# Performance work log

Hardware: AMD Instinct MI355X
Metric: run time of the kernel (lower is better)

The kernel has to match this reference:

```python
import jax, jax.numpy as jnp
import numpy as np

N = 50000
E = 800000
D_IN = 64
D_H = 64


def setup_inputs() -> dict:
    key = jax.random.key(0)
    k1, k2, k3, k4 = jax.random.split(key, 4)
    x = jax.random.normal(k1, (N, D_IN), dtype=jnp.float32)
    edge_index = jax.random.randint(k2, (2, E), 0, N, dtype=jnp.int32)
    W1 = jax.random.normal(k3, (D_IN, D_H), dtype=jnp.float32) * (1.0 / np.sqrt(D_IN))
    b1 = jnp.zeros((D_H,), dtype=jnp.float32)
    W2 = jax.random.normal(k4, (D_H, 1), dtype=jnp.float32) * (1.0 / np.sqrt(D_H))
    b2 = jnpp = jnp.zeros((1,), dtype=jnp.float32)
    return {"x": x, "edge_index": edge_index, "W1": W1, "b1": b1, "W2": W2, "b2": b2}


def reference(x, edge_index, W1, b1, W2, b2):
    n = x.shape[0]
    # dgl.add_self_loop: append (i, i) edges for every node
    loops = jnp.arange(n, dtype=edge_index.dtype)
    src = jnp.concatenate([edge_index[0], loops])
    dst = jnp.concatenate([edge_index[1], loops])

    ones = jnp.ones(src.shape[0], dtype=x.dtype)
    deg_out = jax.ops.segment_sum(ones, src, num_segments=n)  # out-degree (src side)
    deg_in = jax.ops.segment_sum(ones, dst, num_segments=n)   # in-degree (dst side)
    # norm='both': symmetric D^{-1/2} A D^{-1/2}; zero where degree is zero (DGL sets inf->0)
    norm_src = jnp.where(deg_out > 0, jax.lax.rsqrt(deg_out), 0.0)[:, None]
    norm_dst = jnp.where(deg_in > 0, jax.lax.rsqrt(deg_in), 0.0)[:, None]

    def aggregate(h):
        # degree-normalized sparse neighbor sum (SpMM via gather + segment_sum)
        h = h * norm_src
        m = jax.ops.segment_sum(h[src], dst, num_segments=n)
        return m * norm_dst

    # layer 1 (in_feats == h_feats -> aggregate first, then transform), bias after agg
    h = aggregate(x) @ W1 + b1
    h = jax.nn.relu(h)
    # layer 2 (in_feats > out_feats -> transform first, then aggregate), bias at end
    out = aggregate(h @ W2) + b2
    return out  # [N, 1]
```

## Files before the change

kernel.cpp:

```cpp
#include <hip/hip_runtime.h>


constexpr int D = 64;
constexpr int NODE_TILE = 12800;
constexpr int NCHUNK = 64;
constexpr int HTH = 1024;

typedef float f32x8 __attribute__((ext_vector_type(8)));

__device__ __forceinline__ int rl_i(int v, int l) { return __builtin_amdgcn_readlane(v, l); }
__device__ __forceinline__ float rl_f(float v, int l) {
    return __builtin_bit_cast(float, __builtin_amdgcn_readlane(__builtin_bit_cast(int, v), l));
}

__global__ void __launch_bounds__(HTH) k_hist_gemm(
        const int* __restrict__ src, const int* __restrict__ dst,
        unsigned int* __restrict__ part, int e, int ce, int hblocks,
        const float* __restrict__ x, const float* __restrict__ W1,
        float* __restrict__ y, int n) {
    extern __shared__ char smem[];
    int tid = threadIdx.x;

    if (blockIdx.x < (unsigned)hblocks) {
        unsigned int* h = (unsigned int*)smem;
        int b = blockIdx.x & (NCHUNK - 1);
        int pass = blockIdx.x >> 6;
        int v0 = pass * NODE_TILE;
        for (int i = tid; i < NODE_TILE; i += HTH) h[i] = 0u;
        __syncthreads();
        int lo = b * ce, hi = min(lo + ce, e);
        for (int i = lo + tid; i < hi; i += HTH) {
            unsigned int us = (unsigned int)(src[i] - v0);
            if (us < (unsigned int)NODE_TILE) atomicAdd(&h[us], 1u);
            unsigned int ud = (unsigned int)(dst[i] - v0);
            if (ud < (unsigned int)NODE_TILE) atomicAdd(&h[ud], 0x10000u);
        }
        __syncthreads();
        unsigned int* p = part + ((size_t)pass * NCHUNK + b) * NODE_TILE;
        for (int i = tid; i < NODE_TILE; i += HTH) p[i] = h[i];
    } else {
        float* sW1 = (float*)smem;
        for (int i = tid; i < D * D; i += HTH) sW1[i] = W1[i];
        __syncthreads();

        int lane = tid & 63;
        int wv = __builtin_amdgcn_readfirstlane(tid >> 6);
        int gb = blockIdx.x - hblocks;
        int r0 = (gb * 16 + wv) * 8;
        if (r0 >= n) return;

        float acc[8];
#pragma unroll
        for (int i = 0; i < 8; ++i) acc[i] = 0.0f;

        if (r0 + 8 <= n) {
            const float* xw = x + (size_t)r0 * D;
#pragma unroll
            for (int kt = 0; kt < 8; ++kt) {
                const float* p = xw + kt * 8;
                f32x8 X0, X1, X2, X3, X4, X5, X6, X7;
                asm volatile(
                    "s_load_dwordx8 %0, %8, 0x0\n\t"
                    "s_load_dwordx8 %1, %8, 0x100\n\t"
                    "s_load_dwordx8 %2, %8, 0x200\n\t"
                    "s_load_dwordx8 %3, %8, 0x300\n\t"
                    "s_load_dwordx8 %4, %8, 0x400\n\t"
                    "s_load_dwordx8 %5, %8, 0x500\n\t"
                    "s_load_dwordx8 %6, %8, 0x600\n\t"
                    "s_load_dwordx8 %7, %8, 0x700\n\t"
                    "s_waitcnt lgkmcnt(0)"
                    : "=s"(X0), "=s"(X1), "=s"(X2), "=s"(X3),
                      "=s"(X4), "=s"(X5), "=s"(X6), "=s"(X7)
                    : "s"(p));
#pragma unroll
                for (int j = 0; j < 8; ++j) {
                    float wk = sW1[(kt * 8 + j) * D + lane];
                    acc[0] = fmaf(X0[j], wk, acc[0]);
                    acc[1] = fmaf(X1[j], wk, acc[1]);
                    acc[2] = fmaf(X2[j], wk, acc[2]);
                    acc[3] = fmaf(X3[j], wk, acc[3]);
                    acc[4] = fmaf(X4[j], wk, acc[4]);
                    acc[5] = fmaf(X5[j], wk, acc[5]);
                    acc[6] = fmaf(X6[j], wk, acc[6]);
                    acc[7] = fmaf(X7[j], wk, acc[7]);
                }
            }
#pragma unroll
            for (int i = 0; i < 8; ++i)
                y[(size_t)(r0 + i) * D + lane] = acc[i];
        } else {
            float xr[8];
#pragma unroll
            for (int i = 0; i < 8; ++i) {
                int r = r0 + i;
                xr[i] = (r < n) ? x[(size_t)r * D + lane] : 0.0f;
            }
#pragma unroll
            for (int k = 0; k < D; ++k) {
                float wk = sW1[k * D + lane];
#pragma unroll
                for (int i = 0; i < 8; ++i)
                    acc[i] = fmaf(rl_f(xr[i], k), wk, acc[i]);
            }
#pragma unroll
            for (int i = 0; i < 8; ++i) {
                int r = r0 + i;
                if (r < n) y[(size_t)r * D + lane] = acc[i];
            }
        }
    }
}

__global__ void k_merge_scan(const unsigned int* __restrict__ part,
                             unsigned short* __restrict__ colpref,
                             int* __restrict__ cnt_out, int* __restrict__ cnt_in,
                             int* __restrict__ cursor, int* __restrict__ bsum, int n) {
    __shared__ int s[256];
    int tid = threadIdx.x;
    int v = blockIdx.x * 256 + tid;
    int ci = 0;
    if (v < n) {
        int pass = v / NODE_TILE;
        int vl = v - pass * NODE_TILE;
        const unsigned int* p = part + (size_t)pass * NCHUNK * NODE_TILE + vl;
        unsigned int tot = 0, run_in = 0;
        for (int b = 0; b < NCHUNK; ++b) {
            colpref[(size_t)b * n + v] = (unsigned short)run_in;
            unsigned int t = p[(size_t)b * NODE_TILE];
            tot += t;
            run_in += t >> 16;
        }
        cnt_out[v] = (int)(tot & 0xFFFFu);
        ci = (int)(tot >> 16);
        cnt_in[v] = ci;
    }
    s[tid] = ci;
    __syncthreads();
#pragma unroll
    for (int off = 1; off < 256; off <<= 1) {
        int t = (tid >= off) ? s[tid - off] : 0;
        __syncthreads();
        s[tid] += t;
        __syncthreads();
    }
    if (v < n) cursor[v] = s[tid] - ci;
    if (tid == 255) bsum[blockIdx.x] = s[255];
}

__global__ void k_scan_bsum(int* __restrict__ bsum, int nb) {
    __shared__ int s[256];
    __shared__ int carry;
    int tid = threadIdx.x;
    if (tid == 0) carry = 0;
    __syncthreads();
    for (int start = 0; start < nb; start += 256) {
        int i = start + tid;
        int v = (i < nb) ? bsum[i] : 0;
        s[tid] = v;
        __syncthreads();
#pragma unroll
        for (int off = 1; off < 256; off <<= 1) {
            int t = (tid >= off) ? s[tid - off] : 0;
            __syncthreads();
            s[tid] += t;
            __syncthreads();
        }
        if (i < nb) bsum[i] = s[tid] - v + carry;
        __syncthreads();
        if (tid == 0) carry += s[255];
        __syncthreads();
    }
}

__global__ void __launch_bounds__(HTH) k_bin_lds(
        const int* __restrict__ src, const int* __restrict__ dst,
        const int* __restrict__ cursor, const int* __restrict__ bsum,
        const unsigned short* __restrict__ colpref,
        const int* __restrict__ cnt_out, const int* __restrict__ cnt_in,
        unsigned int* __restrict__ col, int4* __restrict__ meta,
        int e, int n, int ce) {
    __shared__ int cur[NODE_TILE];
    int b = blockIdx.x;
    int v0 = blockIdx.y * NODE_TILE;
    int vcnt = min(NODE_TILE, n - v0);
    for (int i = threadIdx.x; i < vcnt; i += HTH) {
        int v = v0 + i;
        int gs = cursor[v] + bsum[v >> 8];
        cur[i] = gs + (int)colpref[(size_t)b * n + v];
        if (b == 0) meta[v] = make_int4(gs, cnt_in[v], cnt_out[v], 0);
    }
    __syncthreads();
    int lo = b * ce, hi = min(lo + ce, e);
    for (int i = lo + threadIdx.x; i < hi; i += HTH) {
        int d = dst[i];
        unsigned int ud = (unsigned int)(d - v0);
        if (ud < (unsigned int)NODE_TILE) {
            int s = src[i];
            int p = atomicAdd(&cur[ud], 1);
            col[p] = (unsigned int)s | ((unsigned int)cnt_out[s] << 16);
        }
    }
}

__global__ void __launch_bounds__(256) k_node(
        const float* __restrict__ y, const int4* __restrict__ meta,
        const unsigned int* __restrict__ col,
        const float* __restrict__ b1, const float* __restrict__ W2,
        float* __restrict__ zs, int n) {
    int tid = threadIdx.x;
    int wave = tid >> 6;
    int lane = tid & 63;
    float b1v = b1[lane];
    float w2v = W2[lane];

    int nwaves = gridDim.x * 4;
    int node = blockIdx.x * 4 + wave;
    if (node >= n) return;
    int4 mt = meta[node];

    while (true) {
        int nxt = node + nwaves;
        int4 mt_nx = make_int4(0, 0, 0, 0);
        if (nxt < n) mt_nx = meta[nxt];

        int base = mt.x;
        int cnt = mt.y;
        float nd = rsqrtf((float)(mt.y + 1));
        float ns = rsqrtf((float)(mt.z + 1));

        float a0 = ns * y[(size_t)node * D + lane];
        float a1 = 0.0f, a2 = 0.0f, a3 = 0.0f;

        for (int b0 = 0; b0 < cnt; b0 += 64) {
            int m = cnt - b0; if (m > 64) m = 64;
            unsigned int cw = (lane < m) ? col[base + b0 + lane] : 0u;
            int idx = (int)(cw & 0xFFFFu);
            float w = rsqrtf((float)(cw >> 16) + 1.0f);
            int j = 0;
            for (; j + 8 <= m; j += 8) {
                int s0 = rl_i(idx, j + 0), s1 = rl_i(idx, j + 1);
                int s2 = rl_i(idx, j + 2), s3 = rl_i(idx, j + 3);
                int s4 = rl_i(idx, j + 4), s5 = rl_i(idx, j + 5);
                int s6 = rl_i(idx, j + 6), s7 = rl_i(idx, j + 7);
                float x0 = y[(size_t)s0 * D + lane];
                float x1 = y[(size_t)s1 * D + lane];
                float x2 = y[(size_t)s2 * D + lane];
                float x3 = y[(size_t)s3 * D + lane];
                float x4 = y[(size_t)s4 * D + lane];
                float x5 = y[(size_t)s5 * D + lane];
                float x6 = y[(size_t)s6 * D + lane];
                float x7 = y[(size_t)s7 * D + lane];
                a0 = fmaf(rl_f(w, j + 0), x0, a0);
                a1 = fmaf(rl_f(w, j + 1), x1, a1);
                a2 = fmaf(rl_f(w, j + 2), x2, a2);
                a3 = fmaf(rl_f(w, j + 3), x3, a3);
                a0 = fmaf(rl_f(w, j + 4), x4, a0);
                a1 = fmaf(rl_f(w, j + 5), x5, a1);
                a2 = fmaf(rl_f(w, j + 6), x6, a2);
                a3 = fmaf(rl_f(w, j + 7), x7, a3);
            }
            for (; j < m; ++j)
                a0 = fmaf(rl_f(w, j), y[(size_t)rl_i(idx, j) * D + lane], a0);
        }

        float h = fmaxf(((a0 + a1) + (a2 + a3)) * nd + b1v, 0.0f);
        float zp = h * w2v;
#pragma unroll
        for (int off = 32; off > 0; off >>= 1) zp += __shfl_down(zp, off);
        if (lane == 0) zs[node] = zp * ns;

        if (nxt >= n) break;
        node = nxt;
        mt = mt_nx;
    }
}

__global__ void k_out(const float* __restrict__ zs,
                      const int4* __restrict__ meta, const unsigned int* __restrict__ col,
                      const float* __restrict__ b2,
                      float* __restrict__ out, int n) {
    int g = blockIdx.x * blockDim.x + threadIdx.x;
    int node = g >> 3;
    int sub = g & 7;
    if (node >= n) return;
    int4 mt = meta[node];
    int base = mt.x;
    int c = mt.y;
    float s = (sub == 0) ? zs[node] : 0.0f;
    for (int j = sub; j < c; j += 8) s += zs[col[base + j] & 0xFFFFu];
    s += __shfl_xor(s, 1);
    s += __shfl_xor(s, 2);
    s += __shfl_xor(s, 4);
    if (sub == 0) {
        float nd = rsqrtf((float)(mt.y + 1));
        out[node] = nd * s + b2[0];
    }
}

extern "C" void kernel_launch(void* const* d_in, const int* in_sizes, int n_in,
                              void* d_out, int out_size, void* d_ws, size_t ws_size,
                              hipStream_t stream) {
    const float* x  = (const float*)d_in[0];
    const int*   ei = (const int*)d_in[1];
    const float* W1 = (const float*)d_in[2];
    const float* b1 = (const float*)d_in[3];
    const float* W2 = (const float*)d_in[4];
    const float* b2 = (const float*)d_in[5];
    float* out = (float*)d_out;

    const int n = in_sizes[0] / D;
    const int e = in_sizes[1] / 2;
    const int* src = ei;
    const int* dst = ei + e;

    const int nb = (n + 255) / 256;
    const int npass = (n + NODE_TILE - 1) / NODE_TILE;
    const int ce = (e + NCHUNK - 1) / NCHUNK;
    const int hblocks = NCHUNK * npass;
    const int gblocks = (n + 127) / 128;

    char* ws = (char*)d_ws;
    int*   cnt_out = (int*)ws;   ws += sizeof(int) * (size_t)n;
    int*   cnt_in  = (int*)ws;   ws += sizeof(int) * (size_t)n;
    int*   cursor  = (int*)ws;   ws += sizeof(int) * (size_t)n;
    int*   bsum    = (int*)ws;   ws += sizeof(int) * (size_t)((nb + 255) & ~255);
    int4*  meta    = (int4*)ws;  ws += sizeof(int4) * (size_t)n;
    unsigned short* colpref = (unsigned short*)ws;
    ws += sizeof(unsigned short) * (size_t)NCHUNK * n;
    unsigned int* col = (unsigned int*)ws;  ws += sizeof(unsigned int) * (size_t)e;
    unsigned int* part = (unsigned int*)ws;
    ws += sizeof(unsigned int) * (size_t)npass * NCHUNK * NODE_TILE;
    float* y  = (float*)ws;      ws += sizeof(float) * (size_t)n * D;
    float* zs = (float*)ws;      ws += sizeof(float) * (size_t)n;

    const int B = 256;
    const size_t smem = (size_t)NODE_TILE * sizeof(unsigned int);

    k_hist_gemm<<<hblocks + gblocks, HTH, smem, stream>>>(
        src, dst, part, e, ce, hblocks, x, W1, y, n);
    k_merge_scan<<<nb, 256, 0, stream>>>(part, colpref, cnt_out, cnt_in, cursor, bsum, n);
    k_scan_bsum<<<1, 256, 0, stream>>>(bsum, nb);
    k_bin_lds<<<dim3(NCHUNK, npass), HTH, 0, stream>>>(
        src, dst, cursor, bsum, colpref, cnt_out, cnt_in, col, meta, e, n, ce);
    k_node<<<2048, B, 0, stream>>>(y, meta, col, b1, W2, zs, n);
    k_out<<<((size_t)n * 8 + B - 1) / B, B, 0, stream>>>(zs, meta, col, b2, out, n);
}
```

Before: 105.6 us.

## Pack two nodes per 32-bit LDS histogram word to cover all nodes in one pass

The per-node histograms now hold two 16-bit counters per 32-bit LDS word, so all 50000 nodes fit in one block's shared memory (about 100KB). This removes the four-pass node tiling that made every chunk rescan all edges once per tile. In/out degree histograms move to separate block sets, and the binning kernel now runs as a single pass that also uses packed 16-bit cursors. The int4 meta array is dropped in favour of packed in/out counts plus cursor+bsum computed on the fly, which adds extra global loads in the node and output kernels and relies on per-chunk counts staying under 65536.

After: 118.1 us. +11.8%, slower.

```diff
diff --git a/kernel.cpp b/kernel.cpp
--- a/kernel.cpp
+++ b/kernel.cpp
@@ -2,7 +2,6 @@
 
 
 constexpr int D = 64;
-constexpr int NODE_TILE = 12800;
 constexpr int NCHUNK = 64;
 constexpr int HTH = 1024;
 
@@ -15,29 +14,28 @@
 
 __global__ void __launch_bounds__(HTH) k_hist_gemm(
         const int* __restrict__ src, const int* __restrict__ dst,
-        unsigned int* __restrict__ part, int e, int ce, int hblocks,
+        unsigned int* __restrict__ part_in, unsigned int* __restrict__ part_out,
+        int e, int ce, int W,
         const float* __restrict__ x, const float* __restrict__ W1,
         float* __restrict__ y, int n) {
-    extern __shared__ char smem[];
+    extern __shared__ unsigned int smem[];
     int tid = threadIdx.x;
 
-    if (blockIdx.x < (unsigned)hblocks) {
-        unsigned int* h = (unsigned int*)smem;
+    if (blockIdx.x < 2 * NCHUNK) {
+        unsigned int* h = smem;
+        int isOut = (blockIdx.x >= NCHUNK) ? 1 : 0;
         int b = blockIdx.x & (NCHUNK - 1);
-        int pass = blockIdx.x >> 6;
-        int v0 = pass * NODE_TILE;
-        for (int i = tid; i < NODE_TILE; i += HTH) h[i] = 0u;
+        const int* key = isOut ? src : dst;
+        for (int i = tid; i < W; i += HTH) h[i] = 0u;
         __syncthreads();
         int lo = b * ce, hi = min(lo + ce, e);
         for (int i = lo + tid; i < hi; i += HTH) {
-            unsigned int us = (unsigned int)(src[i] - v0);
-            if (us < (unsigned int)NODE_TILE) atomicAdd(&h[us], 1u);
-            unsigned int ud = (unsigned int)(dst[i] - v0);
-            if (ud < (unsigned int)NODE_TILE) atomicAdd(&h[ud], 0x10000u);
-        }
-        __syncthreads();
-        unsigned int* p = part + ((size_t)pass * NCHUNK + b) * NODE_TILE;
-        for (int i = tid; i < NODE_TILE; i += HTH) p[i] = h[i];
+            int v = key[i];
+            atomicAdd(&h[v >> 1], (v & 1) ? 0x10000u : 1u);
+        }
+        __syncthreads();
+        unsigned int* p = (isOut ? part_out : part_in) + (size_t)b * W;
+        for (int i = tid; i < W; i += HTH) p[i] = h[i];
     } else {
         float* sW1 = (float*)smem;
         for (int i = tid; i < D * D; i += HTH) sW1[i] = W1[i];
@@ -45,7 +43,7 @@
 
         int lane = tid & 63;
         int wv = __builtin_amdgcn_readfirstlane(tid >> 6);
-        int gb = blockIdx.x - hblocks;
+        int gb = blockIdx.x - 2 * NCHUNK;
         int r0 = (gb * 16 + wv) * 8;
         if (r0 >= n) return;
 
@@ -111,28 +109,27 @@
     }
 }
 
-__global__ void k_merge_scan(const unsigned int* __restrict__ part,
+__global__ void k_merge_scan(const unsigned int* __restrict__ part_in,
+                             const unsigned int* __restrict__ part_out,
                              unsigned short* __restrict__ colpref,
-                             int* __restrict__ cnt_out, int* __restrict__ cnt_in,
-                             int* __restrict__ cursor, int* __restrict__ bsum, int n) {
+                             unsigned int* __restrict__ cnts,
+                             int* __restrict__ cursor, int* __restrict__ bsum,
+                             int n, int W) {
     __shared__ int s[256];
     int tid = threadIdx.x;
     int v = blockIdx.x * 256 + tid;
     int ci = 0;
     if (v < n) {
-        int pass = v / NODE_TILE;
-        int vl = v - pass * NODE_TILE;
-        const unsigned int* p = part + (size_t)pass * NCHUNK * NODE_TILE + vl;
-        unsigned int tot = 0, run_in = 0;
+        int sh = (v & 1) * 16;
+        size_t w = (size_t)(v >> 1);
+        unsigned int run_in = 0, tout = 0;
         for (int b = 0; b < NCHUNK; ++b) {
             colpref[(size_t)b * n + v] = (unsigned short)run_in;
-            unsigned int t = p[(size_t)b * NODE_TILE];
-            tot += t;
-            run_in += t >> 16;
-        }
-        cnt_out[v] = (int)(tot & 0xFFFFu);
-        ci = (int)(tot >> 16);
-        cnt_in[v] = ci;
+            run_in += (part_in[(size_t)b * W + w] >> sh) & 0xFFFFu;
+            tout   += (part_out[(size_t)b * W + w] >> sh) & 0xFFFFu;
+        }
+        ci = (int)run_in;
+        cnts[v] = run_in | (tout << 16);
     }
     s[tid] = ci;
     __syncthreads();
@@ -172,38 +169,32 @@
     }
 }
 
-__global__ void __launch_bounds__(HTH) k_bin_lds(
+__global__ void __launch_bounds__(HTH) k_bin(
         const int* __restrict__ src, const int* __restrict__ dst,
         const int* __restrict__ cursor, const int* __restrict__ bsum,
         const unsigned short* __restrict__ colpref,
-        const int* __restrict__ cnt_out, const int* __restrict__ cnt_in,
-        unsigned int* __restrict__ col, int4* __restrict__ meta,
-        int e, int n, int ce) {
-    __shared__ int cur[NODE_TILE];
+        const unsigned int* __restrict__ cnts,
+        unsigned int* __restrict__ col, int e, int n, int ce, int W) {
+    extern __shared__ unsigned int cur[];
     int b = blockIdx.x;
-    int v0 = blockIdx.y * NODE_TILE;
-    int vcnt = min(NODE_TILE, n - v0);
-    for (int i = threadIdx.x; i < vcnt; i += HTH) {
-        int v = v0 + i;
-        int gs = cursor[v] + bsum[v >> 8];
-        cur[i] = gs + (int)colpref[(size_t)b * n + v];
-        if (b == 0) meta[v] = make_int4(gs, cnt_in[v], cnt_out[v], 0);
-    }
+    const unsigned int* cp = (const unsigned int*)(colpref + (size_t)b * n);
+    for (int i = threadIdx.x; i < W; i += HTH) cur[i] = cp[i];
     __syncthreads();
     int lo = b * ce, hi = min(lo + ce, e);
     for (int i = lo + threadIdx.x; i < hi; i += HTH) {
         int d = dst[i];
-        unsigned int ud = (unsigned int)(d - v0);
-        if (ud < (unsigned int)NODE_TILE) {
-            int s = src[i];
-            int p = atomicAdd(&cur[ud], 1);
-            col[p] = (unsigned int)s | ((unsigned int)cnt_out[s] << 16);
-        }
+        int s2 = src[i];
+        unsigned int old = atomicAdd(&cur[d >> 1], (d & 1) ? 0x10000u : 1u);
+        int pl = (int)((old >> ((d & 1) * 16)) & 0xFFFFu);
+        int p = cursor[d] + bsum[d >> 8] + pl;
+        col[p] = (unsigned int)s2 | (cnts[s2] & 0xFFFF0000u);
     }
 }
 
 __global__ void __launch_bounds__(256) k_node(
-        const float* __restrict__ y, const int4* __restrict__ meta,
+        const float* __restrict__ y,
+        const int* __restrict__ cursor, const int* __restrict__ bsum,
+        const unsigned int* __restrict__ cnts,
         const unsigned int* __restrict__ col,
         const float* __restrict__ b1, const float* __restrict__ W2,
         float* __restrict__ zs, int n) {
@@ -216,17 +207,18 @@
     int nwaves = gridDim.x * 4;
     int node = blockIdx.x * 4 + wave;
     if (node >= n) return;
-    int4 mt = meta[node];
+    int cu = cursor[node];
+    unsigned int cn = cnts[node];
 
     while (true) {
         int nxt = node + nwaves;
-        int4 mt_nx = make_int4(0, 0, 0, 0);
-        if (nxt < n) mt_nx = meta[nxt];
-
-        int base = mt.x;
-        int cnt = mt.y;
-        float nd = rsqrtf((float)(mt.y + 1));
-        float ns = rsqrtf((float)(mt.z + 1));
+        int cu_nx = 0; unsigned int cn_nx = 0;
+        if (nxt < n) { cu_nx = cursor[nxt]; cn_nx = cnts[nxt]; }
+
+        int base = cu + bsum[node >> 8];
+        int cnt = (int)(cn & 0xFFFFu);
+        float nd = rsqrtf((float)(cn & 0xFFFFu) + 1.0f);
+        float ns = rsqrtf((float)(cn >> 16) + 1.0f);
 
         float a0 = ns * y[(size_t)node * D + lane];
         float a1 = 0.0f, a2 = 0.0f, a3 = 0.0f;
@@ -271,28 +263,31 @@
 
         if (nxt >= n) break;
         node = nxt;
-        mt = mt_nx;
+        cu = cu_nx;
+        cn = cn_nx;
     }
 }
 
 __global__ void k_out(const float* __restrict__ zs,
-                      const int4* __restrict__ meta, const unsigned int* __restrict__ col,
+                      const int* __restrict__ cursor, const int* __restrict__ bsum,
+                      const unsigned int* __restrict__ cnts,
+                      const unsigned int* __restrict__ col,
                       const float* __restrict__ b2,
                       float* __restrict__ out, int n) {
     int g = blockIdx.x * blockDim.x + threadIdx.x;
     int node = g >> 3;
     int sub = g & 7;
     if (node >= n) return;
-    int4 mt = meta[node];
-    int base = mt.x;
-    int c = mt.y;
+    unsigned int cn = cnts[node];
+    int base = cursor[node] + bsum[node >> 8];
+    int c = (int)(cn & 0xFFFFu);
     float s = (sub == 0) ? zs[node] : 0.0f;
     for (int j = sub; j < c; j += 8) s += zs[col[base + j] & 0xFFFFu];
     s += __shfl_xor(s, 1);
     s += __shfl_xor(s, 2);
     s += __shfl_xor(s, 4);
     if (sub == 0) {
-        float nd = rsqrtf((float)(mt.y + 1));
+        float nd = rsqrtf((float)(cn & 0xFFFFu) + 1.0f);
         out[node] = nd * s + b2[0];
     }
 }
@@ -314,34 +309,35 @@
     const int* dst = ei + e;
 
     const int nb = (n + 255) / 256;
-    const int npass = (n + NODE_TILE - 1) / NODE_TILE;
     const int ce = (e + NCHUNK - 1) / NCHUNK;
-    const int hblocks = NCHUNK * npass;
+    const int W = (n + 1) / 2;
     const int gblocks = (n + 127) / 128;
 
     char* ws = (char*)d_ws;
-    int*   cnt_out = (int*)ws;   ws += sizeof(int) * (size_t)n;
-    int*   cnt_in  = (int*)ws;   ws += sizeof(int) * (size_t)n;
-    int*   cursor  = (int*)ws;   ws += sizeof(int) * (size_t)n;
-    int*   bsum    = (int*)ws;   ws += sizeof(int) * (size_t)((nb + 255) & ~255);
-    int4*  meta    = (int4*)ws;  ws += sizeof(int4) * (size_t)n;
+    int*   cursor = (int*)ws;    ws += sizeof(int) * (size_t)n;
+    int*   bsum   = (int*)ws;    ws += sizeof(int) * (size_t)((nb + 255) & ~255);
+    unsigned int* cnts = (unsigned int*)ws;  ws += sizeof(unsigned int) * (size_t)n;
     unsigned short* colpref = (unsigned short*)ws;
     ws += sizeof(unsigned short) * (size_t)NCHUNK * n;
-    unsigned int* col = (unsigned int*)ws;  ws += sizeof(unsigned int) * (size_t)e;
-    unsigned int* part = (unsigned int*)ws;
-    ws += sizeof(unsigned int) * (size_t)npass * NCHUNK * NODE_TILE;
+    unsigned int* col = (unsigned int*)ws;   ws += sizeof(unsigned int) * (size_t)e;
+    unsigned int* part_in = (unsigned int*)ws;
+    ws += sizeof(unsigned int) * (size_t)NCHUNK * W;
+    unsigned int* part_out = (unsigned int*)ws;
+    ws += sizeof(unsigned int) * (size_t)NCHUNK * W;
     float* y  = (float*)ws;      ws += sizeof(float) * (size_t)n * D;
     float* zs = (float*)ws;      ws += sizeof(float) * (size_t)n;
 
     const int B = 256;
-    const size_t smem = (size_t)NODE_TILE * sizeof(unsigned int);
-
-    k_hist_gemm<<<hblocks + gblocks, HTH, smem, stream>>>(
-        src, dst, part, e, ce, hblocks, x, W1, y, n);
-    k_merge_scan<<<nb, 256, 0, stream>>>(part, colpref, cnt_out, cnt_in, cursor, bsum, n);
+    const size_t smem = (size_t)W * sizeof(unsigned int);
+
+    k_hist_gemm<<<2 * NCHUNK + gblocks, HTH, smem, stream>>>(
+        src, dst, part_in, part_out, e, ce, W, x, W1, y, n);
+    k_merge_scan<<<nb, 256, 0, stream>>>(part_in, part_out, colpref, cnts,
+                                         cursor, bsum, n, W);
     k_scan_bsum<<<1, 256, 0, stream>>>(bsum, nb);
-    k_bin_lds<<<dim3(NCHUNK, npass), HTH, 0, stream>>>(
-        src, dst, cursor, bsum, colpref, cnt_out, cnt_in, col, meta, e, n, ce);
-    k_node<<<2048, B, 0, stream>>>(y, meta, col, b1, W2, zs, n);
-    k_out<<<((size_t)n * 8 + B - 1) / B, B, 0, stream>>>(zs, meta, col, b2, out, n);
-}
+    k_bin<<<NCHUNK, HTH, smem, stream>>>(src, dst, cursor, bsum, colpref, cnts,
+                                         col, e, n, ce, W);
+    k_node<<<2048, B, 0, stream>>>(y, cursor, bsum, cnts, col, b1, W2, zs, n);
+    k_out<<<((size_t)n * 8 + B - 1) / B, B, 0, stream>>>(zs, cursor, bsum, cnts,
+                                                         col, b2, out, n);
+}
```
